# Kernel optimization log

Measured on AMD Instinct MI355X. Metric: run time of the kernel, lower is better.

## Reference

```python
import jax, jax.numpy as jnp
import numpy as np

VOCAB = 401
E = 256   # embed_size
H = 768   # hidden_size
O = 3     # output_size
B = 64
T = 1024


def setup_inputs() -> dict:
    key = jax.random.key(0)
    ks = jax.random.split(key, 8)
    s = lambda fan_in: 1.0 / np.sqrt(fan_in)
    return {
        "tokens": jax.random.randint(ks[0], (B, T), 0, VOCAB),
        "hidden": jnp.zeros((B, H), dtype=jnp.float32),
        "embed": jax.random.normal(ks[1], (VOCAB, E), dtype=jnp.float32),
        "W_ih": jax.random.uniform(ks[2], (3 * H, E), jnp.float32, -s(H), s(H)),
        "W_hh": jax.random.uniform(ks[3], (3 * H, H), jnp.float32, -s(H), s(H)),
        "b_ih": jax.random.uniform(ks[4], (3 * H,), jnp.float32, -s(H), s(H)),
        "b_hh": jax.random.uniform(ks[5], (3 * H,), jnp.float32, -s(H), s(H)),
        "W_out": jax.random.uniform(ks[6], (O, H), jnp.float32, -s(H), s(H)),
        "b_out": jax.random.uniform(ks[7], (O,), jnp.float32, -s(H), s(H)),
    }


def reference(tokens, hidden, embed, W_ih, W_hh, b_ih, b_hh, W_out, b_out):
    # Embedding lookup for all timesteps: [B, T, E]
    x = embed[tokens]
    # Precompute input-to-hidden projections for all steps: [B, T, 3H]
    xi = jnp.einsum("bte,ge->btg", x, W_ih) + b_ih
    # Note: original forward zeroes the passed-in hidden; we honor that.
    h0 = jnp.zeros_like(hidden)

    def step(h, xt):  # xt: [B, 3H]
        gh = h @ W_hh.T + b_hh                      # [B, 3H]
        xr, xz, xn = jnp.split(xt, 3, axis=1)
        hr, hz, hn = jnp.split(gh, 3, axis=1)
        r = jax.nn.sigmoid(xr + hr)
        z = jax.nn.sigmoid(xz + hz)
        n = jnp.tanh(xn + r * hn)
        h_new = (1.0 - z) * n + z * h
        return h_new, None

    h_final, _ = jax.lax.scan(step, h0, jnp.swapaxes(xi, 0, 1))  # scan over T
    logits = h_final @ W_out.T + b_out                            # [B, O]
    logprobs = jax.nn.log_softmax(logits, axis=1)
    return (logprobs, h_final)
```

## Files before the change

kernel.cpp:

```cpp
#include <hip/hip_runtime.h>

#define VOCABN 401
#define EN 256
#define HN 768
#define H3N 2304
#define ON 3
#define BN 64
#define TN 1024

#define NREP 16
#define WGPR 16
#define BPR  4
#define JPW  48
#define NTH  768

typedef _Float16 f16x8 __attribute__((ext_vector_type(8)));
typedef float f32x4 __attribute__((ext_vector_type(4)));
typedef unsigned long long u64;

__device__ __forceinline__ void barrier_lgkm() {
    asm volatile("s_waitcnt lgkmcnt(0)\n\ts_barrier" ::: "memory");
}

__global__ __launch_bounds__(256)
void k_build_gtab(const float* __restrict__ embed, const float* __restrict__ wih,
                  const float* __restrict__ bih, float* __restrict__ gtab) {
    const int g  = blockIdx.x * 64 + (threadIdx.x >> 2);
    const int ql = threadIdx.x & 3;
    const int v0 = blockIdx.y * 26;
    const int v1 = min(VOCABN, v0 + 26);
    float4 w[16];
    const float4* s4 = (const float4*)(wih + (size_t)g * EN + ql * 64);
#pragma unroll
    for (int i = 0; i < 16; ++i) w[i] = s4[i];
    const float bias = bih[g];
    for (int v = v0; v < v1; ++v) {
        const float4* e4 = (const float4*)(embed + (size_t)v * EN + ql * 64);
        float acc = 0.f;
#pragma unroll
        for (int i = 0; i < 16; ++i) {
            float4 e = e4[i];
            acc += w[i].x * e.x + w[i].y * e.y + w[i].z * e.z + w[i].w * e.w;
        }
        acc += __shfl_xor(acc, 1, 64);
        acc += __shfl_xor(acc, 2, 64);
        if (ql == 0) gtab[(size_t)v * H3N + g] = acc + bias;
    }
}

__global__ __launch_bounds__(NTH, 1)
void k_rnn(const int* __restrict__ tokens, const float* __restrict__ whh,
           const float* __restrict__ gtab, const float* __restrict__ bhh,
           unsigned* __restrict__ hbuf, float* __restrict__ hout) {
    const int R    = blockIdx.x & (NREP - 1);
    const int wg   = blockIdx.x >> 4;
    const int tid  = threadIdx.x;
    const int lane = tid & 63;
    const int wave = tid >> 6;
    const int wr   = wave % 3;
    const int wk   = wave / 3;
    const int koff8 = ((lane >> 4) & 3) * 8;
    const int kbase = wk * 192;

    __shared__ __align__(16) _Float16 hT[BPR * HN];
    __shared__ __align__(16) float psum[4][144];

    f16x8 a[3][6];
#pragma unroll
    for (int tt = 0; tt < 3; ++tt) {
        const int lr  = wr * 48 + tt * 16 + (lane & 15);
        const int g   = lr / 48;
        const int jlr = lr % 48;
        const float* wsrc = whh + (size_t)(g * HN + wg * JPW + jlr) * HN;
#pragma unroll
        for (int ks = 0; ks < 6; ++ks) {
            const float4* p4 = (const float4*)(wsrc + kbase + ks * 32 + koff8);
            float4 x0 = p4[0], x1 = p4[1];
            f16x8 t;
            t[0] = (_Float16)x0.x; t[1] = (_Float16)x0.y;
            t[2] = (_Float16)x0.z; t[3] = (_Float16)x0.w;
            t[4] = (_Float16)x1.x; t[5] = (_Float16)x1.y;
            t[6] = (_Float16)x1.z; t[7] = (_Float16)x1.w;
            a[tt][ks] = t;
        }
    }

    u64* hb2 = (u64*)hbuf + (size_t)R * (2 * BPR * 384);

    const int gt    = tid - 576;
    const int bown  = (gt >= 0) ? gt / 48 : 0;
    const int jlown = (gt >= 0) ? gt - bown * 48 : 0;
    const int jown  = wg * JPW + jlown;
    float hprev = 0.f, xr = 0.f, xz = 0.f, xn = 0.f, bhr = 0.f, bhz = 0.f, bhn = 0.f;
    if (gt >= 0) {
        bhr = bhh[jown]; bhz = bhh[HN + jown]; bhn = bhh[2 * HN + jown];
        const int tok = tokens[(size_t)(R * BPR + bown) * TN + 0];
        const float* g_ = gtab + (size_t)tok * H3N;
        xr = g_[jown]; xz = g_[HN + jown]; xn = g_[2 * HN + jown];
    }

    u64 vin = 0;
    if (tid < 384)
        vin = __hip_atomic_load(hb2 + tid, __ATOMIC_RELAXED, __HIP_MEMORY_SCOPE_AGENT);

#pragma unroll 1
    for (int t = 0; t < TN; ++t) {
        const u64 want_pair = ((u64)(unsigned)t << 16) | ((u64)(unsigned)t << 48);
#pragma unroll
        for (int b = 0; b < BPR; ++b) {
            if (tid < 384) {
                const u64* cur = hb2 + ((t & 1) * BPR + b) * 384 + tid;
                while ((vin & 0xFFFF0000FFFF0000ull) != want_pair) {
                    __builtin_amdgcn_s_sleep(1);
                    vin = __hip_atomic_load(cur, __ATOMIC_RELAXED, __HIP_MEMORY_SCOPE_AGENT);
                }
                ((unsigned*)hT)[b * 384 + tid] =
                    __builtin_amdgcn_perm((unsigned)(vin >> 32), (unsigned)vin, 0x05040100);
                int b1 = b + 1;
                const int t1 = t + (b1 >> 2);
                b1 &= 3;
                if (t1 < TN)
                    vin = __hip_atomic_load(hb2 + ((t1 & 1) * BPR + b1) * 384 + tid,
                                            __ATOMIC_RELAXED, __HIP_MEMORY_SCOPE_AGENT);
            }
            barrier_lgkm();

            {
                f32x4 acc0 = {0.f, 0.f, 0.f, 0.f};
                f32x4 acc1 = {0.f, 0.f, 0.f, 0.f};
                f32x4 acc2 = {0.f, 0.f, 0.f, 0.f};
#pragma unroll
                for (int ks = 0; ks < 6; ++ks) {
                    f16x8 bf = *(const f16x8*)(hT + b * HN + kbase + ks * 32 + koff8);
                    acc0 = __builtin_amdgcn_mfma_f32_16x16x32_f16(a[0][ks], bf, acc0, 0, 0, 0);
                    acc1 = __builtin_amdgcn_mfma_f32_16x16x32_f16(a[1][ks], bf, acc1, 0, 0, 0);
                    acc2 = __builtin_amdgcn_mfma_f32_16x16x32_f16(a[2][ks], bf, acc2, 0, 0, 0);
                }
                if ((lane & 15) == 0) {
                    const int r0 = wr * 48 + ((lane >> 4) & 3) * 4;
                    *(f32x4*)&psum[wk][r0]      = acc0;
                    *(f32x4*)&psum[wk][r0 + 16] = acc1;
                    *(f32x4*)&psum[wk][r0 + 32] = acc2;
                }
            }
            barrier_lgkm();

            if (gt >= 0 && bown == b) {
                const float sr = (psum[0][jlown]      + psum[1][jlown])
                               + (psum[2][jlown]      + psum[3][jlown]);
                const float sz = (psum[0][48 + jlown] + psum[1][48 + jlown])
                               + (psum[2][48 + jlown] + psum[3][48 + jlown]);
                const float sn = (psum[0][96 + jlown] + psum[1][96 + jlown])
                               + (psum[2][96 + jlown] + psum[3][96 + jlown]);
                const float r  = 1.f / (1.f + __expf(-(xr + sr + bhr)));
                const float z  = 1.f / (1.f + __expf(-(xz + sz + bhz)));
                const float nx = xn + r * (sn + bhn);
                const float n  = 1.f - 2.f / (__expf(2.f * nx) + 1.f);
                hprev = (1.f - z) * n + z * hprev;
                unsigned pk = ((unsigned)(t + 1) << 16)
                    | (unsigned)__builtin_bit_cast(unsigned short, (_Float16)hprev);
                const unsigned pk2 = __shfl_down(pk, 1, 64);
                if (t < TN - 1) {
                    if (!(jlown & 1))
                        __hip_atomic_store(
                            hb2 + (((t + 1) & 1) * BPR + b) * 384 + wg * 24 + (jlown >> 1),
                            (u64)pk | ((u64)pk2 << 32),
                            __ATOMIC_RELAXED, __HIP_MEMORY_SCOPE_AGENT);
                    const int tok = tokens[(size_t)(R * BPR + bown) * TN + (t + 1)];
                    const float* g_ = gtab + (size_t)tok * H3N;
                    xr = g_[jown]; xz = g_[HN + jown]; xn = g_[2 * HN + jown];
                } else {
                    hout[(size_t)(R * BPR + bown) * HN + jown] = hprev;
                }
            }
        }
    }
}

__global__ void k_logits(const float* __restrict__ hfin, const float* __restrict__ wout,
                         const float* __restrict__ bout, float* __restrict__ lp) {
    const int b = blockIdx.x;
    const int o = threadIdx.x / 64;
    const int lane = threadIdx.x % 64;
    const float* hrow = hfin + (size_t)b * HN;
    const float* w = wout + (size_t)o * HN;
    float p = 0.f;
    for (int k = lane; k < HN; k += 64) p += hrow[k] * w[k];
    for (int off = 32; off > 0; off >>= 1) p += __shfl_down(p, off, 64);
    __shared__ float lg[ON];
    if (lane == 0) lg[o] = p + bout[o];
    __syncthreads();
    if (threadIdx.x == 0) {
        float m = fmaxf(lg[0], fmaxf(lg[1], lg[2]));
        float s = __expf(lg[0] - m) + __expf(lg[1] - m) + __expf(lg[2] - m);
        float ls = __logf(s);
        lp[b * ON + 0] = lg[0] - m - ls;
        lp[b * ON + 1] = lg[1] - m - ls;
        lp[b * ON + 2] = lg[2] - m - ls;
    }
}

extern "C" void kernel_launch(void* const* d_in, const int* in_sizes, int n_in,
                              void* d_out, int out_size, void* d_ws, size_t ws_size,
                              hipStream_t stream) {
    const int*   tokens = (const int*)d_in[0];
    const float* embed  = (const float*)d_in[2];
    const float* wih    = (const float*)d_in[3];
    const float* whh    = (const float*)d_in[4];
    const float* bih    = (const float*)d_in[5];
    const float* bhh    = (const float*)d_in[6];
    const float* wout   = (const float*)d_in[7];
    const float* bout   = (const float*)d_in[8];

    float* out = (float*)d_out;
    char* ws = (char*)d_ws;
    const size_t GTAB_OFF = 0;
    const size_t HBUF_OFF = 3695616;
    float*    gtab = (float*)(ws + GTAB_OFF);
    unsigned* hbuf = (unsigned*)(ws + HBUF_OFF);

    hipMemsetAsync(ws + HBUF_OFF, 0, 393216, stream);

    hipLaunchKernelGGL(k_build_gtab, dim3(H3N / 64, 16), dim3(256), 0, stream,
                       embed, wih, bih, gtab);
    hipLaunchKernelGGL(k_rnn, dim3(NREP * WGPR), dim3(NTH), 0, stream,
                       tokens, whh, gtab, bhh, hbuf, out + BN * ON);
    hipLaunchKernelGGL(k_logits, dim3(BN), dim3(192), 0, stream,
                       out + BN * ON, wout, bout, out);
}
```

Measured before the change: 5.506 ms.

## Software-pipeline GRU gate stage two steps behind MFMA, one barrier per stage

Flattens the time and batch loops into one stage loop. Each stage polls and loads the hidden vector for batch s, runs the gate update for stage s-2, then issues a single barrier before the MFMA matvec. psum is now buffered per batch slot, so the gate math reads older partial sums while new ones are written. This halves the workgroup barriers per step and overlaps the gate and atomic publish with the polling. The cost is four times the psum LDS and more intricate index and dependency bookkeeping.

```diff
diff --git a/kernel.cpp b/kernel.cpp
--- a/kernel.cpp
+++ b/kernel.cpp
@@ -62,8 +62,8 @@
     const int koff8 = ((lane >> 4) & 3) * 8;
     const int kbase = wk * 192;
 
-    __shared__ __align__(16) _Float16 hT[BPR * HN];
-    __shared__ __align__(16) float psum[4][144];
+    __shared__ __align__(16) _Float16 hT[BPR][HN];
+    __shared__ __align__(16) float psum[BPR][4][144];
 
     f16x8 a[3][6];
 #pragma unroll
@@ -103,75 +103,77 @@
     if (tid < 384)
         vin = __hip_atomic_load(hb2 + tid, __ATOMIC_RELAXED, __HIP_MEMORY_SCOPE_AGENT);
 
+    const int NSTG = TN * 4 + 2;
 #pragma unroll 1
-    for (int t = 0; t < TN; ++t) {
-        const u64 want_pair = ((u64)(unsigned)t << 16) | ((u64)(unsigned)t << 48);
-#pragma unroll
-        for (int b = 0; b < BPR; ++b) {
-            if (tid < 384) {
-                const u64* cur = hb2 + ((t & 1) * BPR + b) * 384 + tid;
-                while ((vin & 0xFFFF0000FFFF0000ull) != want_pair) {
-                    __builtin_amdgcn_s_sleep(1);
-                    vin = __hip_atomic_load(cur, __ATOMIC_RELAXED, __HIP_MEMORY_SCOPE_AGENT);
-                }
-                ((unsigned*)hT)[b * 384 + tid] =
-                    __builtin_amdgcn_perm((unsigned)(vin >> 32), (unsigned)vin, 0x05040100);
-                int b1 = b + 1;
-                const int t1 = t + (b1 >> 2);
-                b1 &= 3;
-                if (t1 < TN)
-                    vin = __hip_atomic_load(hb2 + ((t1 & 1) * BPR + b1) * 384 + tid,
-                                            __ATOMIC_RELAXED, __HIP_MEMORY_SCOPE_AGENT);
-            }
-            barrier_lgkm();
-
-            {
-                f32x4 acc0 = {0.f, 0.f, 0.f, 0.f};
-                f32x4 acc1 = {0.f, 0.f, 0.f, 0.f};
-                f32x4 acc2 = {0.f, 0.f, 0.f, 0.f};
-#pragma unroll
-                for (int ks = 0; ks < 6; ++ks) {
-                    f16x8 bf = *(const f16x8*)(hT + b * HN + kbase + ks * 32 + koff8);
-                    acc0 = __builtin_amdgcn_mfma_f32_16x16x32_f16(a[0][ks], bf, acc0, 0, 0, 0);
-                    acc1 = __builtin_amdgcn_mfma_f32_16x16x32_f16(a[1][ks], bf, acc1, 0, 0, 0);
-                    acc2 = __builtin_amdgcn_mfma_f32_16x16x32_f16(a[2][ks], bf, acc2, 0, 0, 0);
-                }
-                if ((lane & 15) == 0) {
-                    const int r0 = wr * 48 + ((lane >> 4) & 3) * 4;
-                    *(f32x4*)&psum[wk][r0]      = acc0;
-                    *(f32x4*)&psum[wk][r0 + 16] = acc1;
-                    *(f32x4*)&psum[wk][r0 + 32] = acc2;
-                }
-            }
-            barrier_lgkm();
-
-            if (gt >= 0 && bown == b) {
-                const float sr = (psum[0][jlown]      + psum[1][jlown])
-                               + (psum[2][jlown]      + psum[3][jlown]);
-                const float sz = (psum[0][48 + jlown] + psum[1][48 + jlown])
-                               + (psum[2][48 + jlown] + psum[3][48 + jlown]);
-                const float sn = (psum[0][96 + jlown] + psum[1][96 + jlown])
-                               + (psum[2][96 + jlown] + psum[3][96 + jlown]);
+    for (int s = 0; s < NSTG; ++s) {
+        const int b  = s & 3;
+        const int ts = s >> 2;
+
+        if (s < TN * 4 && tid < 384) {
+            const u64 want = ((u64)(unsigned)ts << 16) | ((u64)(unsigned)ts << 48);
+            const u64* cur = hb2 + ((ts & 1) * BPR + b) * 384 + tid;
+            while ((vin & 0xFFFF0000FFFF0000ull) != want) {
+                __builtin_amdgcn_s_sleep(1);
+                vin = __hip_atomic_load(cur, __ATOMIC_RELAXED, __HIP_MEMORY_SCOPE_AGENT);
+            }
+            ((unsigned*)hT)[b * 384 + tid] =
+                __builtin_amdgcn_perm((unsigned)(vin >> 32), (unsigned)vin, 0x05040100);
+            const int s1 = s + 1;
+            if (s1 < TN * 4) {
+                const int b1 = s1 & 3, t1 = s1 >> 2;
+                vin = __hip_atomic_load(hb2 + ((t1 & 1) * BPR + b1) * 384 + tid,
+                                        __ATOMIC_RELAXED, __HIP_MEMORY_SCOPE_AGENT);
+            }
+        }
+        if (gt >= 0 && s >= 2) {
+            const int gs = s - 2, gb = gs & 3, tg = gs >> 2;
+            if (bown == gb) {
+                const float sr = (psum[gb][0][jlown]      + psum[gb][1][jlown])
+                               + (psum[gb][2][jlown]      + psum[gb][3][jlown]);
+                const float sz = (psum[gb][0][48 + jlown] + psum[gb][1][48 + jlown])
+                               + (psum[gb][2][48 + jlown] + psum[gb][3][48 + jlown]);
+                const float sn = (psum[gb][0][96 + jlown] + psum[gb][1][96 + jlown])
+                               + (psum[gb][2][96 + jlown] + psum[gb][3][96 + jlown]);
                 const float r  = 1.f / (1.f + __expf(-(xr + sr + bhr)));
                 const float z  = 1.f / (1.f + __expf(-(xz + sz + bhz)));
                 const float nx = xn + r * (sn + bhn);
                 const float n  = 1.f - 2.f / (__expf(2.f * nx) + 1.f);
                 hprev = (1.f - z) * n + z * hprev;
-                unsigned pk = ((unsigned)(t + 1) << 16)
+                unsigned pk = ((unsigned)(tg + 1) << 16)
                     | (unsigned)__builtin_bit_cast(unsigned short, (_Float16)hprev);
                 const unsigned pk2 = __shfl_down(pk, 1, 64);
-                if (t < TN - 1) {
+                if (tg < TN - 1) {
                     if (!(jlown & 1))
                         __hip_atomic_store(
-                            hb2 + (((t + 1) & 1) * BPR + b) * 384 + wg * 24 + (jlown >> 1),
+                            hb2 + (((tg + 1) & 1) * BPR + gb) * 384 + wg * 24 + (jlown >> 1),
                             (u64)pk | ((u64)pk2 << 32),
                             __ATOMIC_RELAXED, __HIP_MEMORY_SCOPE_AGENT);
-                    const int tok = tokens[(size_t)(R * BPR + bown) * TN + (t + 1)];
+                    const int tok = tokens[(size_t)(R * BPR + bown) * TN + (tg + 1)];
                     const float* g_ = gtab + (size_t)tok * H3N;
                     xr = g_[jown]; xz = g_[HN + jown]; xn = g_[2 * HN + jown];
                 } else {
                     hout[(size_t)(R * BPR + bown) * HN + jown] = hprev;
                 }
+            }
+        }
+        barrier_lgkm();
+
+        if (s < TN * 4) {
+            f32x4 acc0 = {0.f, 0.f, 0.f, 0.f};
+            f32x4 acc1 = {0.f, 0.f, 0.f, 0.f};
+            f32x4 acc2 = {0.f, 0.f, 0.f, 0.f};
+#pragma unroll
+            for (int ks = 0; ks < 6; ++ks) {
+                f16x8 bf = *(const f16x8*)(&hT[b][kbase + ks * 32 + koff8]);
+                acc0 = __builtin_amdgcn_mfma_f32_16x16x32_f16(a[0][ks], bf, acc0, 0, 0, 0);
+                acc1 = __builtin_amdgcn_mfma_f32_16x16x32_f16(a[1][ks], bf, acc1, 0, 0, 0);
+                acc2 = __builtin_amdgcn_mfma_f32_16x16x32_f16(a[2][ks], bf, acc2, 0, 0, 0);
+            }
+            if ((lane & 15) == 0) {
+                const int r0 = wr * 48 + (lane >> 4) * 4;
+                *(f32x4*)&psum[b][wk][r0]      = acc0;
+                *(f32x4*)&psum[b][wk][r0 + 16] = acc1;
+                *(f32x4*)&psum[b][wk][r0 + 32] = acc2;
             }
         }
     }
```

After: 5.607 ms. Within noise of the previous version (+1.8%).

## Restructure GRU recurrence: full-K waves, 8 batches per replica, single barrier per step

Applied to the files above, without the earlier changes.

The recurrent kernel is repartitioned into 8 replicas of 12 workgroups, each handling 8 batch rows. Each wave now owns 16 hidden units across the full 768-wide K dimension, so it holds all three gates' weights in registers and no longer needs the cross-wave shared-memory partial-sum reduction or the second barrier. Gate math now runs directly on the MFMA accumulator lanes. Tokens are staged in LDS, the h-buffer and gtab values for the next batch are prefetched into double buffers, and the previous hidden state is read back as fp16 from shared memory rather than kept in fp32. In exchange the weights take very heavy register pressure, the dependent MFMA chain per batch is much longer, batches are processed more serially, and the fp16 carry slightly changes precision.

```diff
diff --git a/kernel.cpp b/kernel.cpp
--- a/kernel.cpp
+++ b/kernel.cpp
@@ -8,11 +8,10 @@
 #define BN 64
 #define TN 1024
 
-#define NREP 16
-#define WGPR 16
-#define BPR  4
-#define JPW  48
-#define NTH  768
+#define NREP 8
+#define WGR  12
+#define BPR  8
+#define NTH  256
 
 typedef _Float16 f16x8 __attribute__((ext_vector_type(8)));
 typedef float f32x4 __attribute__((ext_vector_type(4)));
@@ -53,124 +52,138 @@
            const float* __restrict__ gtab, const float* __restrict__ bhh,
            unsigned* __restrict__ hbuf, float* __restrict__ hout) {
     const int R    = blockIdx.x & (NREP - 1);
-    const int wg   = blockIdx.x >> 4;
+    const int wgj  = blockIdx.x >> 3;
     const int tid  = threadIdx.x;
     const int lane = tid & 63;
-    const int wave = tid >> 6;
-    const int wr   = wave % 3;
-    const int wk   = wave / 3;
-    const int koff8 = ((lane >> 4) & 3) * 8;
-    const int kbase = wk * 192;
-
-    __shared__ __align__(16) _Float16 hT[BPR * HN];
-    __shared__ __align__(16) float psum[4][144];
-
-    f16x8 a[3][6];
-#pragma unroll
-    for (int tt = 0; tt < 3; ++tt) {
-        const int lr  = wr * 48 + tt * 16 + (lane & 15);
-        const int g   = lr / 48;
-        const int jlr = lr % 48;
-        const float* wsrc = whh + (size_t)(g * HN + wg * JPW + jlr) * HN;
-#pragma unroll
-        for (int ks = 0; ks < 6; ++ks) {
-            const float4* p4 = (const float4*)(wsrc + kbase + ks * 32 + koff8);
+    const int jb   = tid >> 6;
+    const int j_tile = wgj * 64 + jb * 16;
+    const int rowl = lane & 15;
+    const int kg   = lane >> 4;
+    const int jx   = j_tile + kg * 4;
+
+    __shared__ int stok[BPR][TN];
+    __shared__ __align__(16) _Float16 hT[2][HN];
+
+    for (int i = tid; i < BPR * TN; i += NTH)
+        stok[i >> 10][i & 1023] = tokens[(size_t)(R * BPR + (i >> 10)) * TN + (i & 1023)];
+
+    f16x8 a[3][24];
+#pragma unroll
+    for (int g = 0; g < 3; ++g) {
+        const float* wsrc = whh + (size_t)(g * HN + j_tile + rowl) * HN;
+#pragma unroll
+        for (int ks = 0; ks < 24; ++ks) {
+            const float4* p4 = (const float4*)(wsrc + ks * 32 + kg * 8);
             float4 x0 = p4[0], x1 = p4[1];
-            f16x8 t;
-            t[0] = (_Float16)x0.x; t[1] = (_Float16)x0.y;
-            t[2] = (_Float16)x0.z; t[3] = (_Float16)x0.w;
-            t[4] = (_Float16)x1.x; t[5] = (_Float16)x1.y;
-            t[6] = (_Float16)x1.z; t[7] = (_Float16)x1.w;
-            a[tt][ks] = t;
+            f16x8 tf;
+            tf[0]=(_Float16)x0.x; tf[1]=(_Float16)x0.y; tf[2]=(_Float16)x0.z; tf[3]=(_Float16)x0.w;
+            tf[4]=(_Float16)x1.x; tf[5]=(_Float16)x1.y; tf[6]=(_Float16)x1.z; tf[7]=(_Float16)x1.w;
+            a[g][ks] = tf;
         }
     }
+    const float4 bR = *(const float4*)(bhh + jx);
+    const float4 bZ = *(const float4*)(bhh + HN + jx);
+    const float4 bN = *(const float4*)(bhh + 2 * HN + jx);
 
     u64* hb2 = (u64*)hbuf + (size_t)R * (2 * BPR * 384);
 
-    const int gt    = tid - 576;
-    const int bown  = (gt >= 0) ? gt / 48 : 0;
-    const int jlown = (gt >= 0) ? gt - bown * 48 : 0;
-    const int jown  = wg * JPW + jlown;
-    float hprev = 0.f, xr = 0.f, xz = 0.f, xn = 0.f, bhr = 0.f, bhz = 0.f, bhn = 0.f;
-    if (gt >= 0) {
-        bhr = bhh[jown]; bhz = bhh[HN + jown]; bhn = bhh[2 * HN + jown];
-        const int tok = tokens[(size_t)(R * BPR + bown) * TN + 0];
+    u64 v[2][3] = {0, 0, 0, 0, 0, 0};
+    float4 xR[2], xZ[2], xN[2];
+    xR[0] = xR[1] = xZ[0] = xZ[1] = xN[0] = xN[1] = float4{0, 0, 0, 0};
+
+    if (tid < 128) {
+#pragma unroll
+        for (int q = 0; q < 3; ++q)
+            v[0][q] = __hip_atomic_load(hb2 + 3 * tid + q,
+                                        __ATOMIC_RELAXED, __HIP_MEMORY_SCOPE_AGENT);
+    }
+    __syncthreads();
+    {
+        const int tok = stok[0][0];
         const float* g_ = gtab + (size_t)tok * H3N;
-        xr = g_[jown]; xz = g_[HN + jown]; xn = g_[2 * HN + jown];
-    }
-
-    u64 vin = 0;
-    if (tid < 384)
-        vin = __hip_atomic_load(hb2 + tid, __ATOMIC_RELAXED, __HIP_MEMORY_SCOPE_AGENT);
+        xR[0] = *(const float4*)(g_ + jx);
+        xZ[0] = *(const float4*)(g_ + HN + jx);
+        xN[0] = *(const float4*)(g_ + 2 * HN + jx);
+    }
 
 #pragma unroll 1
     for (int t = 0; t < TN; ++t) {
-        const u64 want_pair = ((u64)(unsigned)t << 16) | ((u64)(unsigned)t << 48);
-#pragma unroll
-        for (int b = 0; b < BPR; ++b) {
-            if (tid < 384) {
-                const u64* cur = hb2 + ((t & 1) * BPR + b) * 384 + tid;
-                while ((vin & 0xFFFF0000FFFF0000ull) != want_pair) {
-                    __builtin_amdgcn_s_sleep(1);
-                    vin = __hip_atomic_load(cur, __ATOMIC_RELAXED, __HIP_MEMORY_SCOPE_AGENT);
+        const u64 want = ((u64)(unsigned)t << 16) | ((u64)(unsigned)t << 48);
+#pragma unroll 2
+        for (int b8 = 0; b8 < BPR; ++b8) {
+            const int sp = b8 & 1, sn = sp ^ 1;
+            if (tid < 128) {
+#pragma unroll
+                for (int q = 0; q < 3; ++q) {
+                    const u64* cur = hb2 + (t & 1) * 3072 + b8 * 384 + 3 * tid + q;
+                    u64 vv = v[sp][q];
+                    while ((vv & 0xFFFF0000FFFF0000ull) != want) {
+                        __builtin_amdgcn_s_sleep(1);
+                        vv = __hip_atomic_load(cur, __ATOMIC_RELAXED, __HIP_MEMORY_SCOPE_AGENT);
+                    }
+                    ((unsigned*)hT[sp])[3 * tid + q] =
+                        __builtin_amdgcn_perm((unsigned)(vv >> 32), (unsigned)vv, 0x05040100);
                 }
-                ((unsigned*)hT)[b * 384 + tid] =
-                    __builtin_amdgcn_perm((unsigned)(vin >> 32), (unsigned)vin, 0x05040100);
-                int b1 = b + 1;
-                const int t1 = t + (b1 >> 2);
-                b1 &= 3;
-                if (t1 < TN)
-                    vin = __hip_atomic_load(hb2 + ((t1 & 1) * BPR + b1) * 384 + tid,
-                                            __ATOMIC_RELAXED, __HIP_MEMORY_SCOPE_AGENT);
+            }
+            int b1 = b8 + 1;
+            const int t1 = t + (b1 >> 3);
+            b1 &= 7;
+            if (t1 < TN) {
+                if (tid < 128) {
+#pragma unroll
+                    for (int q = 0; q < 3; ++q)
+                        v[sn][q] = __hip_atomic_load(
+                            hb2 + (t1 & 1) * 3072 + b1 * 384 + 3 * tid + q,
+                            __ATOMIC_RELAXED, __HIP_MEMORY_SCOPE_AGENT);
+                }
+                const int tok = stok[b1][t1];
+                const float* g_ = gtab + (size_t)tok * H3N;
+                xR[sn] = *(const float4*)(g_ + jx);
+                xZ[sn] = *(const float4*)(g_ + HN + jx);
+                xN[sn] = *(const float4*)(g_ + 2 * HN + jx);
             }
             barrier_lgkm();
 
-            {
-                f32x4 acc0 = {0.f, 0.f, 0.f, 0.f};
-                f32x4 acc1 = {0.f, 0.f, 0.f, 0.f};
-                f32x4 acc2 = {0.f, 0.f, 0.f, 0.f};
-#pragma unroll
-                for (int ks = 0; ks < 6; ++ks) {
-                    f16x8 bf = *(const f16x8*)(hT + b * HN + kbase + ks * 32 + koff8);
-                    acc0 = __builtin_amdgcn_mfma_f32_16x16x32_f16(a[0][ks], bf, acc0, 0, 0, 0);
-                    acc1 = __builtin_amdgcn_mfma_f32_16x16x32_f16(a[1][ks], bf, acc1, 0, 0, 0);
-                    acc2 = __builtin_amdgcn_mfma_f32_16x16x32_f16(a[2][ks], bf, acc2, 0, 0, 0);
-                }
-                if ((lane & 15) == 0) {
-                    const int r0 = wr * 48 + ((lane >> 4) & 3) * 4;
-                    *(f32x4*)&psum[wk][r0]      = acc0;
-                    *(f32x4*)&psum[wk][r0 + 16] = acc1;
-                    *(f32x4*)&psum[wk][r0 + 32] = acc2;
-                }
-            }
-            barrier_lgkm();
-
-            if (gt >= 0 && bown == b) {
-                const float sr = (psum[0][jlown]      + psum[1][jlown])
-                               + (psum[2][jlown]      + psum[3][jlown]);
-                const float sz = (psum[0][48 + jlown] + psum[1][48 + jlown])
-                               + (psum[2][48 + jlown] + psum[3][48 + jlown]);
-                const float sn = (psum[0][96 + jlown] + psum[1][96 + jlown])
-                               + (psum[2][96 + jlown] + psum[3][96 + jlown]);
-                const float r  = 1.f / (1.f + __expf(-(xr + sr + bhr)));
-                const float z  = 1.f / (1.f + __expf(-(xz + sz + bhz)));
-                const float nx = xn + r * (sn + bhn);
-                const float n  = 1.f - 2.f / (__expf(2.f * nx) + 1.f);
-                hprev = (1.f - z) * n + z * hprev;
-                unsigned pk = ((unsigned)(t + 1) << 16)
-                    | (unsigned)__builtin_bit_cast(unsigned short, (_Float16)hprev);
-                const unsigned pk2 = __shfl_down(pk, 1, 64);
+            f32x4 ar = {0, 0, 0, 0}, az = {0, 0, 0, 0}, an = {0, 0, 0, 0};
+#pragma unroll
+            for (int ks = 0; ks < 24; ++ks) {
+                f16x8 bf = *(const f16x8*)(&hT[sp][ks * 32 + kg * 8]);
+                ar = __builtin_amdgcn_mfma_f32_16x16x32_f16(a[0][ks], bf, ar, 0, 0, 0);
+                az = __builtin_amdgcn_mfma_f32_16x16x32_f16(a[1][ks], bf, az, 0, 0, 0);
+                an = __builtin_amdgcn_mfma_f32_16x16x32_f16(a[2][ks], bf, an, 0, 0, 0);
+            }
+            const _Float16* hop = &hT[sp][jx];
+            unsigned pk[4];
+            float hnewf[4];
+#pragma unroll
+            for (int r = 0; r < 4; ++r) {
+                const float sr = ar[r] + ((const float*)&bR)[r];
+                const float sz = az[r] + ((const float*)&bZ)[r];
+                const float sn_ = an[r] + ((const float*)&bN)[r];
+                const float xr = ((const float*)&xR[sp])[r];
+                const float xz = ((const float*)&xZ[sp])[r];
+                const float xn = ((const float*)&xN[sp])[r];
+                const float rr = 1.f / (1.f + __expf(-(xr + sr)));
+                const float zz = 1.f / (1.f + __expf(-(xz + sz)));
+                const float nx = xn + rr * sn_;
+                const float nn = 1.f - 2.f / (__expf(2.f * nx) + 1.f);
+                const float ho = (float)hop[r];
+                const float hn = (1.f - zz) * nn + zz * ho;
+                hnewf[r] = hn;
+                pk[r] = ((unsigned)(t + 1) << 16)
+                      | (unsigned)__builtin_bit_cast(unsigned short, (_Float16)hn);
+            }
+            if ((lane & 15) == 0) {
                 if (t < TN - 1) {
-                    if (!(jlown & 1))
-                        __hip_atomic_store(
-                            hb2 + (((t + 1) & 1) * BPR + b) * 384 + wg * 24 + (jlown >> 1),
-                            (u64)pk | ((u64)pk2 << 32),
-                            __ATOMIC_RELAXED, __HIP_MEMORY_SCOPE_AGENT);
-                    const int tok = tokens[(size_t)(R * BPR + bown) * TN + (t + 1)];
-                    const float* g_ = gtab + (size_t)tok * H3N;
-                    xr = g_[jown]; xz = g_[HN + jown]; xn = g_[2 * HN + jown];
+                    u64* dst = hb2 + ((t + 1) & 1) * 3072 + b8 * 384 + (jx >> 1);
+                    __hip_atomic_store(dst,     (u64)pk[0] | ((u64)pk[1] << 32),
+                                       __ATOMIC_RELAXED, __HIP_MEMORY_SCOPE_AGENT);
+                    __hip_atomic_store(dst + 1, (u64)pk[2] | ((u64)pk[3] << 32),
+                                       __ATOMIC_RELAXED, __HIP_MEMORY_SCOPE_AGENT);
                 } else {
-                    hout[(size_t)(R * BPR + bown) * HN + jown] = hprev;
+                    float* ho_ = hout + (size_t)(R * BPR + b8) * HN + jx;
+                    ho_[0] = hnewf[0]; ho_[1] = hnewf[1];
+                    ho_[2] = hnewf[2]; ho_[3] = hnewf[3];
                 }
             }
         }
@@ -223,7 +236,7 @@
 
     hipLaunchKernelGGL(k_build_gtab, dim3(H3N / 64, 16), dim3(256), 0, stream,
                        embed, wih, bih, gtab);
-    hipLaunchKernelGGL(k_rnn, dim3(NREP * WGPR), dim3(NTH), 0, stream,
+    hipLaunchKernelGGL(k_rnn, dim3(NREP * WGR), dim3(NTH), 0, stream,
                        tokens, whh, gtab, bhh, hbuf, out + BN * ON);
     hipLaunchKernelGGL(k_logits, dim3(BN), dim3(192), 0, stream,
                        out + BN * ON, wout, bout, out);
```

After: 16.64 ms. +202.3%, slower.
